# Kernel optimization log

Hardware: AMD Instinct MI355X
Metric: run time of the kernel (lower is better)

Reference implementation:

```python
import jax, jax.numpy as jnp
import numpy as np

NODES = 163842
IN_FEATS = 32
OUT_FEATS = 64

def setup_inputs() -> dict:
    key = jax.random.key(0)
    k1, k2, k3, k4, k5 = jax.random.split(key, 5)
    x = jax.random.normal(k1, (NODES, IN_FEATS), dtype=jnp.float32)
    # 0-based neighbor indices (original stores 1-based and subtracts 1)
    neigh_indices = jax.random.randint(k2, (NODES, 25, 3), 0, NODES, dtype=jnp.int32)
    # barycentric interpolation weights per (node, 25 template positions, 3 triangle verts)
    neigh_weights = jax.random.uniform(k3, (NODES, 25, 3), dtype=jnp.float32)
    W = jax.random.normal(k4, (OUT_FEATS, 25 * IN_FEATS), dtype=jnp.float32) * 0.02
    b = jax.random.normal(k5, (OUT_FEATS,), dtype=jnp.float32) * 0.02
    return {"x": x, "neigh_indices": neigh_indices, "neigh_weights": neigh_weights, "W": W, "b": b}

def reference(x, neigh_indices, neigh_weights, W, b):
    nodes, c = x.shape
    # gather neighbor features: (nodes, 25, 3, in_feats)
    mat = x[neigh_indices.reshape(-1)].reshape(nodes, 25, 3, c)
    # barycentric weighted sum over the 3 triangle vertices -> (nodes, 25, in_feats)
    feat = jnp.sum(mat * neigh_weights[..., None], axis=2)
    # flatten the 25 template positions and project: (nodes, out_feats)
    feat = feat.reshape(nodes, 25 * c)
    return feat @ W.T + b
```

## Files before the change

### kernel.cpp

```cpp
#include <hip/hip_runtime.h>
#include <hip/hip_bf16.h>

#define NNODES   163842
#define INF      32
#define OUTF     64
#define NPOS     25
#define KTOT     800
#define MT       64
#define NTHREADS 256

typedef float  f32x4  __attribute__((ext_vector_type(4)));
typedef __bf16 bf16x8 __attribute__((ext_vector_type(8)));
typedef __bf16 bf16x4 __attribute__((ext_vector_type(4)));

__global__ void cvt_kernel(const float* __restrict__ x, const float* __restrict__ W,
                           __bf16* __restrict__ xb, __bf16* __restrict__ wb) {
    int tid = blockIdx.x * blockDim.x + threadIdx.x;
    int stride = gridDim.x * blockDim.x;
    const f32x4* x4 = (const f32x4*)x;
    bf16x4* xb4 = (bf16x4*)xb;
    const int nx4 = NNODES * INF / 4;
    for (int j = tid; j < nx4; j += stride) {
        f32x4 v = x4[j];
        bf16x4 o;
        #pragma unroll
        for (int k = 0; k < 4; ++k) o[k] = (__bf16)v[k];
        xb4[j] = o;
    }
    const f32x4* w4 = (const f32x4*)W;
    bf16x4* wb4 = (bf16x4*)wb;
    const int nw4 = OUTF * KTOT / 4;
    for (int j = tid; j < nw4; j += stride) {
        f32x4 v = w4[j];
        bf16x4 o;
        #pragma unroll
        for (int k = 0; k < 4; ++k) o[k] = (__bf16)v[k];
        wb4[j] = o;
    }
}

__launch_bounds__(NTHREADS, 1)
__global__ void conv_mfma(const int* __restrict__ nidx, const float* __restrict__ nwt,
                          const __bf16* __restrict__ xb, const __bf16* __restrict__ wb,
                          const float* __restrict__ bias, float* __restrict__ out) {
    __shared__ int   idxs[MT * 75];
    __shared__ float wts [MT * 75];

    const int tid = threadIdx.x;
    const int blk = blockIdx.x;

    {
        const long gbase = (long)blk * (MT * 75);
        const long tot   = (long)NNODES * 75;
        #pragma unroll
        for (int it = 0; it < (MT * 75 + NTHREADS - 1) / NTHREADS; ++it) {
            int i = tid + it * NTHREADS;
            if (i < MT * 75) {
                long g = gbase + i;
                bool ok = g < tot;
                idxs[i] = ok ? nidx[g] : 0;
                wts [i] = ok ? nwt [g] : 0.0f;
            }
        }
    }

    const int lane = tid & 63;
    const int wave = tid >> 6;
    const int arow = lane & 15;
    const int kgrp = lane >> 4;
    const int gc   = kgrp * 8;
    const int lrow = (wave * 16 + arow) * 75;
    const int base = blk * MT + wave * 16;

    __syncthreads();

    f32x4 acc[4] = {{0,0,0,0},{0,0,0,0},{0,0,0,0},{0,0,0,0}};
    bf16x8 va[15], vb[15];

    auto GATHER = [&](bf16x8 (&v)[15], int g) {
        #pragma unroll
        for (int t = 0; t < 15; ++t) {
            const int idx = idxs[lrow + g * 15 + t];
            v[t] = *(const bf16x8*)(xb + (long)idx * INF + gc);
        }
    };

    auto COMPUTE = [&](const bf16x8 (&v)[15], int g) {
        float w[15];
        #pragma unroll
        for (int t = 0; t < 15; ++t) w[t] = wts[lrow + g * 15 + t];
        #pragma unroll
        for (int p = 0; p < 5; ++p) {
            bf16x8 af;
            #pragma unroll
            for (int j = 0; j < 8; ++j)
                af[j] = (__bf16)(w[p*3+0] * (float)v[p*3+0][j]
                               + w[p*3+1] * (float)v[p*3+1][j]
                               + w[p*3+2] * (float)v[p*3+2][j]);
            const int koff = (g * 5 + p) * INF + gc;
            #pragma unroll
            for (int nb = 0; nb < 4; ++nb) {
                bf16x8 bw = *(const bf16x8*)(wb + (16*nb + arow) * KTOT + koff);
                acc[nb] = __builtin_amdgcn_mfma_f32_16x16x32_bf16(af, bw, acc[nb], 0, 0, 0);
            }
        }
    };

    GATHER(va, 0);
    GATHER(vb, 1);
    COMPUTE(va, 0);
    GATHER(va, 2);
    COMPUTE(vb, 1);
    GATHER(vb, 3);
    COMPUTE(va, 2);
    GATHER(va, 4);
    COMPUTE(vb, 3);
    COMPUTE(va, 4);

    #pragma unroll
    for (int nb = 0; nb < 4; ++nb) {
        const int col = 16*nb + arow;
        const float bv = bias[col];
        #pragma unroll
        for (int r = 0; r < 4; ++r) {
            const int row = base + 4*kgrp + r;
            if (row < NNODES) out[(long)row * OUTF + col] = acc[nb][r] + bv;
        }
    }
}

__global__ void conv_fallback(const float* __restrict__ x, const int* __restrict__ nidx,
                              const float* __restrict__ nwt, const float* __restrict__ W,
                              const float* __restrict__ bias, float* __restrict__ out) {
    __shared__ float feat[KTOT];
    const int n = blockIdx.x;
    const int t = threadIdx.x;
    for (int e = t; e < KTOT; e += 64) {
        const int p = e >> 5, c = e & 31;
        const int ib = n * 75 + p * 3;
        float a = 0.0f;
        #pragma unroll
        for (int v = 0; v < 3; ++v)
            a += nwt[ib+v] * x[nidx[ib+v] * INF + c];
        feat[e] = a;
    }
    __syncthreads();
    float a = bias[t];
    const float* wr = W + t * KTOT;
    for (int k = 0; k < KTOT; ++k) a += feat[k] * wr[k];
    out[(long)n * OUTF + t] = a;
}

extern "C" void kernel_launch(void* const* d_in, const int* in_sizes, int n_in,
                              void* d_out, int out_size, void* d_ws, size_t ws_size,
                              hipStream_t stream) {
    const float* x    = (const float*)d_in[0];
    const int*   nidx = (const int*)  d_in[1];
    const float* nwt  = (const float*)d_in[2];
    const float* W    = (const float*)d_in[3];
    const float* bias = (const float*)d_in[4];
    float* out = (float*)d_out;

    const size_t need = (size_t)NNODES * INF * 2 + (size_t)OUTF * KTOT * 2;
    if (ws_size < need) {
        conv_fallback<<<NNODES, 64, 0, stream>>>(x, nidx, nwt, W, bias, out);
        return;
    }

    __bf16* xb = (__bf16*)d_ws;
    __bf16* wb = xb + (size_t)NNODES * INF;

    cvt_kernel<<<1024, NTHREADS, 0, stream>>>(x, W, xb, wb);
    const int nblocks = (NNODES + MT - 1) / MT;
    conv_mfma<<<nblocks, NTHREADS, 0, stream>>>(nidx, nwt, xb, wb, bias, out);
}
```

Baseline: 183.5 us.

## Switch to fp16 packed math, pre-swizzle W fragments, finer-grained gather/MFMA pipeline

Converts x and W to fp16 instead of bf16 and performs the barycentric blend with packed fp16 vector math, dropping the per-element float conversions. W is pre-laid-out in MFMA fragment order so each lane does one coalesced 16-byte load per fragment, and those W loads are double-buffered alongside the gather. The pipeline moves from 5 groups of 5 positions to 9 groups of 3, separated by sched_barriers, and the launch bound now allows 2 blocks per CU. MFMA operands are swapped so the output is written with vectorized f32x4 stores. Risks include fp16 range and precision loss, and register pressure from the larger prefetch buffers.

```diff
diff --git a/kernel.cpp b/kernel.cpp
--- a/kernel.cpp
+++ b/kernel.cpp
@@ -1,5 +1,6 @@
 #include <hip/hip_runtime.h>
 #include <hip/hip_bf16.h>
+#include <type_traits>
 
 #define NNODES   163842
 #define INF      32
@@ -9,42 +10,44 @@
 #define MT       64
 #define NTHREADS 256
 
-typedef float  f32x4  __attribute__((ext_vector_type(4)));
-typedef __bf16 bf16x8 __attribute__((ext_vector_type(8)));
-typedef __bf16 bf16x4 __attribute__((ext_vector_type(4)));
+typedef float    f32x4 __attribute__((ext_vector_type(4)));
+typedef _Float16 f16x8 __attribute__((ext_vector_type(8)));
 
 __global__ void cvt_kernel(const float* __restrict__ x, const float* __restrict__ W,
-                           __bf16* __restrict__ xb, __bf16* __restrict__ wb) {
+                           _Float16* __restrict__ xh, _Float16* __restrict__ wh) {
     int tid = blockIdx.x * blockDim.x + threadIdx.x;
     int stride = gridDim.x * blockDim.x;
+    const int nx8 = NNODES * INF / 8;
     const f32x4* x4 = (const f32x4*)x;
-    bf16x4* xb4 = (bf16x4*)xb;
-    const int nx4 = NNODES * INF / 4;
-    for (int j = tid; j < nx4; j += stride) {
-        f32x4 v = x4[j];
-        bf16x4 o;
+    f16x8* xh8 = (f16x8*)xh;
+    for (int j = tid; j < nx8; j += stride) {
+        f32x4 a = x4[2*j], b = x4[2*j+1];
+        f16x8 o;
         #pragma unroll
-        for (int k = 0; k < 4; ++k) o[k] = (__bf16)v[k];
-        xb4[j] = o;
+        for (int k = 0; k < 4; ++k) { o[k] = (_Float16)a[k]; o[4+k] = (_Float16)b[k]; }
+        xh8[j] = o;
     }
-    const f32x4* w4 = (const f32x4*)W;
-    bf16x4* wb4 = (bf16x4*)wb;
-    const int nw4 = OUTF * KTOT / 4;
-    for (int j = tid; j < nw4; j += stride) {
-        f32x4 v = w4[j];
-        bf16x4 o;
+    f16x8* wh8 = (f16x8*)wh;
+    for (int t = tid; t < NPOS * 4 * 64; t += stride) {
+        const int l  = t & 63;
+        const int nb = (t >> 6) & 3;
+        const int p  = t >> 8;
+        const int row = 16*nb + (l & 15);
+        const int kb  = p*32 + (l >> 4)*8;
+        const float* src = W + row * KTOT + kb;
+        f16x8 o;
         #pragma unroll
-        for (int k = 0; k < 4; ++k) o[k] = (__bf16)v[k];
-        wb4[j] = o;
+        for (int j = 0; j < 8; ++j) o[j] = (_Float16)src[j];
+        wh8[t] = o;
     }
 }
 
-__launch_bounds__(NTHREADS, 1)
+__launch_bounds__(NTHREADS, 2)
 __global__ void conv_mfma(const int* __restrict__ nidx, const float* __restrict__ nwt,
-                          const __bf16* __restrict__ xb, const __bf16* __restrict__ wb,
+                          const _Float16* __restrict__ xh, const _Float16* __restrict__ wh,
                           const float* __restrict__ bias, float* __restrict__ out) {
-    __shared__ int   idxs[MT * 75];
-    __shared__ float wts [MT * 75];
+    __shared__ int      idxs[MT * 75];
+    __shared__ _Float16 wtsl[MT * 76];
 
     const int tid = threadIdx.x;
     const int blk = blockIdx.x;
@@ -58,8 +61,9 @@
             if (i < MT * 75) {
                 long g = gbase + i;
                 bool ok = g < tot;
+                int n = i / 75, t = i % 75;
                 idxs[i] = ok ? nidx[g] : 0;
-                wts [i] = ok ? nwt [g] : 0.0f;
+                wtsl[n * 76 + t] = ok ? (_Float16)nwt[g] : (_Float16)0.0f;
             }
         }
     }
@@ -68,65 +72,78 @@
     const int wave = tid >> 6;
     const int arow = lane & 15;
     const int kgrp = lane >> 4;
-    const int gc   = kgrp * 8;
-    const int lrow = (wave * 16 + arow) * 75;
-    const int base = blk * MT + wave * 16;
+    const int irow = (wave * 16 + arow) * 75;
+    const int wrow = (wave * 16 + arow) * 76;
+    const int node0 = blk * MT + wave * 16;
+    const _Float16* xg = xh + kgrp * 8;
 
     __syncthreads();
 
     f32x4 acc[4] = {{0,0,0,0},{0,0,0,0},{0,0,0,0},{0,0,0,0}};
-    bf16x8 va[15], vb[15];
+    f16x8 gA[9], gB[9];
+    f16x8 bA[12], bB[12];
 
-    auto GATHER = [&](bf16x8 (&v)[15], int g) {
+    #define SB() __builtin_amdgcn_sched_barrier(0)
+
+    auto BLD = [&](f16x8* b, int g, auto CNT) {
+        constexpr int C = decltype(CNT)::value;
         #pragma unroll
-        for (int t = 0; t < 15; ++t) {
-            const int idx = idxs[lrow + g * 15 + t];
-            v[t] = *(const bf16x8*)(xb + (long)idx * INF + gc);
+        for (int q = 0; q < 4 * C; ++q) {
+            const int f = g * 12 + q;
+            b[q] = *(const f16x8*)(wh + (long)f * 512 + lane * 8);
+        }
+    };
+    auto GATH = [&](f16x8* v, int g, auto CNT) {
+        constexpr int C = decltype(CNT)::value;
+        #pragma unroll
+        for (int t = 0; t < 3 * C; ++t) {
+            const int idx = idxs[irow + g * 9 + t];
+            v[t] = *(const f16x8*)(xg + (long)idx * INF);
+        }
+    };
+    auto COMP = [&](const f16x8* v, const f16x8* b, int g, auto CNT) {
+        constexpr int C = decltype(CNT)::value;
+        #pragma unroll
+        for (int p = 0; p < C; ++p) {
+            const int pos = g * 3 + p;
+            const _Float16 w0 = wtsl[wrow + pos*3 + 0];
+            const _Float16 w1 = wtsl[wrow + pos*3 + 1];
+            const _Float16 w2 = wtsl[wrow + pos*3 + 2];
+            f16x8 af = v[p*3+0] * w0 + v[p*3+1] * w1 + v[p*3+2] * w2;
+            #pragma unroll
+            for (int nb = 0; nb < 4; ++nb)
+                acc[nb] = __builtin_amdgcn_mfma_f32_16x16x32_f16(b[p*4+nb], af, acc[nb], 0, 0, 0);
         }
     };
 
-    auto COMPUTE = [&](const bf16x8 (&v)[15], int g) {
-        float w[15];
+    constexpr std::integral_constant<int,3> C3{};
+    constexpr std::integral_constant<int,1> C1{};
+
+    BLD(bA,0,C3); GATH(gA,0,C3); SB();
+    BLD(bB,1,C3); GATH(gB,1,C3); SB();
+    COMP(gA,bA,0,C3); SB(); BLD(bA,2,C3); GATH(gA,2,C3); SB();
+    COMP(gB,bB,1,C3); SB(); BLD(bB,3,C3); GATH(gB,3,C3); SB();
+    COMP(gA,bA,2,C3); SB(); BLD(bA,4,C3); GATH(gA,4,C3); SB();
+    COMP(gB,bB,3,C3); SB(); BLD(bB,5,C3); GATH(gB,5,C3); SB();
+    COMP(gA,bA,4,C3); SB(); BLD(bA,6,C3); GATH(gA,6,C3); SB();
+    COMP(gB,bB,5,C3); SB(); BLD(bB,7,C3); GATH(gB,7,C3); SB();
+    COMP(gA,bA,6,C3); SB(); BLD(bA,8,C1); GATH(gA,8,C1); SB();
+    COMP(gB,bB,7,C3); SB();
+    COMP(gA,bA,8,C1);
+
+    const int node = node0 + arow;
+    if (node < NNODES) {
         #pragma unroll
-        for (int t = 0; t < 15; ++t) w[t] = wts[lrow + g * 15 + t];
-        #pragma unroll
-        for (int p = 0; p < 5; ++p) {
-            bf16x8 af;
+        for (int nb = 0; nb < 4; ++nb) {
+            const int cb = 16*nb + 4*kgrp;
+            const f32x4 b4 = *(const f32x4*)(bias + cb);
+            f32x4 o;
             #pragma unroll
-            for (int j = 0; j < 8; ++j)
-                af[j] = (__bf16)(w[p*3+0] * (float)v[p*3+0][j]
-                               + w[p*3+1] * (float)v[p*3+1][j]
-                               + w[p*3+2] * (float)v[p*3+2][j]);
-            const int koff = (g * 5 + p) * INF + gc;
-            #pragma unroll
-            for (int nb = 0; nb < 4; ++nb) {
-                bf16x8 bw = *(const bf16x8*)(wb + (16*nb + arow) * KTOT + koff);
-                acc[nb] = __builtin_amdgcn_mfma_f32_16x16x32_bf16(af, bw, acc[nb], 0, 0, 0);
-            }
-        }
-    };
-
-    GATHER(va, 0);
-    GATHER(vb, 1);
-    COMPUTE(va, 0);
-    GATHER(va, 2);
-    COMPUTE(vb, 1);
-    GATHER(vb, 3);
-    COMPUTE(va, 2);
-    GATHER(va, 4);
-    COMPUTE(vb, 3);
-    COMPUTE(va, 4);
-
-    #pragma unroll
-    for (int nb = 0; nb < 4; ++nb) {
-        const int col = 16*nb + arow;
-        const float bv = bias[col];
-        #pragma unroll
-        for (int r = 0; r < 4; ++r) {
-            const int row = base + 4*kgrp + r;
-            if (row < NNODES) out[(long)row * OUTF + col] = acc[nb][r] + bv;
+            for (int r = 0; r < 4; ++r) o[r] = acc[nb][r] + b4[r];
+            *(f32x4*)(out + (long)node * OUTF + cb) = o;
         }
     }
+    #undef SB
 }
 
 __global__ void conv_fallback(const float* __restrict__ x, const int* __restrict__ nidx,
@@ -161,16 +178,16 @@
     const float* bias = (const float*)d_in[4];
     float* out = (float*)d_out;
 
-    const size_t need = (size_t)NNODES * INF * 2 + (size_t)OUTF * KTOT * 2;
+    const size_t need = (size_t)NNODES * INF * 2 + (size_t)NPOS * 4 * 64 * 8 * 2;
     if (ws_size < need) {
         conv_fallback<<<NNODES, 64, 0, stream>>>(x, nidx, nwt, W, bias, out);
         return;
     }
 
-    __bf16* xb = (__bf16*)d_ws;
-    __bf16* wb = xb + (size_t)NNODES * INF;
+    _Float16* xh = (_Float16*)d_ws;
+    _Float16* wh = xh + (size_t)NNODES * INF;
 
-    cvt_kernel<<<1024, NTHREADS, 0, stream>>>(x, W, xb, wb);
+    cvt_kernel<<<1024, NTHREADS, 0, stream>>>(x, W, xh, wh);
     const int nblocks = (NNODES + MT - 1) / MT;
-    conv_mfma<<<nblocks, NTHREADS, 0, stream>>>(nidx, nwt, xb, wb, bias, out);
+    conv_mfma<<<nblocks, NTHREADS, 0, stream>>>(nidx, nwt, xh, wh, bias, out);
 }
```

After: 179.3 us. 1.02x faster.
